# Optimization experiments

Measured on AMD Instinct MI355X. Metric: run time of the kernel, lower is better.

The kernel has to match this reference:

```python
import jax, jax.numpy as jnp
import numpy as np

EPS = 1e-7
MAX_NORM = 1.0 - 1e-3  # projection radius of the unit Poincare ball (c=1)
ALPHA = 0.2            # LeakyReLU negative slope
NEG_INF = -9e15


def _proj(x, max_norm=MAX_NORM):
    # Project points back inside the Poincare ball along the last dim.
    norm = jnp.clip(jnp.linalg.norm(x, axis=-1, keepdims=True), EPS)
    return jnp.where(norm > max_norm, x / norm * max_norm, x)


def _logmap0(x):
    # Log map at the origin of the Poincare ball, c = 1.
    norm = jnp.clip(jnp.linalg.norm(x, axis=-1, keepdims=True), EPS, 1.0 - EPS)
    return jnp.arctanh(norm) * x / norm


def _expmap0(v):
    # Exp map at the origin of the Poincare ball, c = 1.
    norm = jnp.clip(jnp.linalg.norm(v, axis=-1, keepdims=True), EPS)
    return jnp.tanh(norm) * v / norm


def setup_inputs() -> dict:
    key = jax.random.key(0)
    k1, k2, k3 = jax.random.split(key, 3)
    N, D = 12288, 128
    # points strictly inside the ball: ||x|| ~ 0.01*sqrt(128) ~ 0.11 < 1
    x = jax.random.normal(k1, (N, D), dtype=jnp.float32) * 0.01
    adj = jax.random.randint(k2, (N, N), 0, 2, dtype=jnp.int32)
    # attention vector a, as in init: N(0, 0.2) then proj(a, 0.9) row-wise
    a = jax.random.normal(k3, (2 * D, 1), dtype=jnp.float32) * 0.2
    a = _proj(a, 0.9)
    return {"x": x, "adj": adj, "a": a}


def reference(x, adj, a):
    D = a.shape[0] // 2
    x_tan = _logmap0(x)                       # [N, D]
    wh1 = x_tan @ a[:D]                       # [N, 1]
    wh2 = x_tan @ a[D:]                       # [N, 1]
    e = jax.nn.leaky_relu(wh1 + wh2.T, ALPHA)  # [N, N] additive scores
    scores = jnp.where(adj > 0, e, NEG_INF)
    attention = jax.nn.softmax(scores, axis=1)  # dropout omitted (eval mode)
    x_tan_prime = attention @ x_tan            # [N, D]
    return _proj(_expmap0(x_tan_prime))
```

## Files before the change

kernel.cpp:

```cpp
#include <hip/hip_runtime.h>
#include <math.h>

#define NN 12288
#define DD 128
#define EPSF 1e-7f
#define MAXNORM (1.0f - 1e-3f)
#define CSPLIT 4
#define CCOLS (NN / CSPLIT)
#define CSTEPS (CCOLS / 128)
#define BITS_U64_PER_ROW (NN / 64)

typedef __attribute__((ext_vector_type(8))) short short8_t;
typedef __attribute__((ext_vector_type(4))) float float4_t;
typedef unsigned short ushort_t;
typedef unsigned long long u64_t;

__device__ __forceinline__ unsigned short f2bf(float f) {
    unsigned int u = __builtin_bit_cast(unsigned int, f);
    unsigned int r = u + 0x7FFFu + ((u >> 16) & 1u);
    return (unsigned short)(r >> 16);
}

__global__ __launch_bounds__(128) void prep_kernel(
    const float* __restrict__ x, const float* __restrict__ a,
    ushort_t* __restrict__ xtb,
    float* __restrict__ wh1, float* __restrict__ wh2)
{
    const int r = blockIdx.x;
    const int t = threadIdx.x;
    const float xv = x[r * DD + t];
    const float a1 = a[t];
    const float a2 = a[DD + t];
    float s0 = xv * xv, s1 = xv * a1, s2 = xv * a2;
    #pragma unroll
    for (int o = 32; o > 0; o >>= 1) {
        s0 += __shfl_xor(s0, o);
        s1 += __shfl_xor(s1, o);
        s2 += __shfl_xor(s2, o);
    }
    __shared__ float red[6];
    const int w = t >> 6;
    if ((t & 63) == 0) { red[w * 3 + 0] = s0; red[w * 3 + 1] = s1; red[w * 3 + 2] = s2; }
    __syncthreads();
    const float sumsq = red[0] + red[3];
    const float d1    = red[1] + red[4];
    const float d2    = red[2] + red[5];
    const float nraw  = sqrtf(sumsq);
    const float nrm   = fminf(fmaxf(nraw, EPSF), 1.0f - EPSF);
    const float scale = atanhf(nrm) / nrm;
    xtb[(size_t)r * DD + t] = f2bf(xv * scale);
    if (t == 0) {
        wh1[r] = scale * d1;
        wh2[r] = scale * d2;
    }
}

__global__ __launch_bounds__(256) void swizzle_kernel(
    const ushort_t* __restrict__ xtb, ushort_t* __restrict__ xtB)
{
    __shared__ ushort_t raw[32 * 136];
    const int C = blockIdx.x;
    const int t = threadIdx.x;
    #pragma unroll
    for (int p = 0; p < 2; ++p) {
        const int idx = p * 256 + t;
        const int j = idx >> 4, cell = idx & 15;
        const uint4 v = *(const uint4*)(xtb + (size_t)(C * 32 + j) * DD + cell * 8);
        *(uint4*)&raw[j * 136 + cell * 8] = v;
    }
    __syncthreads();
    #pragma unroll
    for (int p = 0; p < 2; ++p) {
        const int oc = p * 256 + t;
        const int dt = oc >> 6;
        const int l6 = oc & 63;
        const int l15 = l6 & 15, q = l6 >> 4;
        short8_t v;
        #pragma unroll
        for (int e = 0; e < 8; ++e)
            v[e] = (short)raw[(q * 8 + e) * 136 + dt * 16 + l15];
        *(short8_t*)(xtB + (size_t)C * 4096 + oc * 8) = v;
    }
}

__global__ __launch_bounds__(256) void bitify_kernel(
    const int* __restrict__ adj, u64_t* __restrict__ bits)
{
    const int i = blockIdx.x;
    const int w = threadIdx.x >> 6;
    const int lane = threadIdx.x & 63;
    const int* rp = adj + (size_t)i * NN;
    #pragma unroll 8
    for (int k = 0; k < BITS_U64_PER_ROW / 4; ++k) {
        const int word = w * (BITS_U64_PER_ROW / 4) + k;
        const int v = rp[word * 64 + lane];
        const u64_t b = __ballot(v > 0);
        if (lane == 0) bits[(size_t)i * BITS_U64_PER_ROW + word] = b;
    }
}

__global__ __launch_bounds__(256, 3) void attn_kernel(
    const u64_t* __restrict__ bits,
    const ushort_t* __restrict__ xtB,
    const float* __restrict__ wh1, const float* __restrict__ wh2,
    float* __restrict__ pout, float* __restrict__ plsum)
{
    __shared__ __align__(16) float wh2_lds[CCOLS];

    const int t = threadIdx.x;
    const int w = t >> 6, lane = t & 63;
    const int l15 = lane & 15, quad = lane >> 4;
    const int cy = blockIdx.y;
    const int jcol0 = cy * CCOLS;
    const int rowbase = blockIdx.x * 64 + w * 16;

    #pragma unroll
    for (int m = 0; m < CCOLS / 256; ++m)
        wh2_lds[m * 256 + t] = wh2[jcol0 + m * 256 + t];
    const float wh1i = wh1[rowbase + l15];
    __syncthreads();

    const uint4* bitp = (const uint4*)bits
                      + (size_t)(rowbase + l15) * (NN / 128) + cy * CSTEPS;
    const ushort_t* Bbase = xtB + (size_t)(jcol0 >> 5) * 4096 + (size_t)lane * 8;

    float4_t acc[8];
    #pragma unroll
    for (int dt = 0; dt < 8; ++dt) acc[dt] = (float4_t)0.0f;
    float lsum = 0.0f;

    auto process = [&](int st, const uint4& A) {
        const int sb = st * 128;
        #pragma unroll
        for (int kc = 0; kc < 4; ++kc) {
            const unsigned word = (kc == 0) ? A.x : (kc == 1) ? A.y
                                : (kc == 2) ? A.z : A.w;
            const unsigned wq = (word >> (quad * 8)) & 0xFFu;
            const int wbase = sb + kc * 32 + quad * 8;
            const float4 Wa = *(const float4*)&wh2_lds[wbase];
            const float4 Wb = *(const float4*)&wh2_lds[wbase + 4];
            const float u0 = wh1i + Wa.x, u1 = wh1i + Wa.y;
            const float u2 = wh1i + Wa.z, u3 = wh1i + Wa.w;
            const float u4 = wh1i + Wb.x, u5 = wh1i + Wb.y;
            const float u6 = wh1i + Wb.z, u7 = wh1i + Wb.w;
            const float p0 = (wq & 1u)   ? __expf(fmaxf(u0, 0.2f * u0)) : 0.0f;
            const float p1 = (wq & 2u)   ? __expf(fmaxf(u1, 0.2f * u1)) : 0.0f;
            const float p2 = (wq & 4u)   ? __expf(fmaxf(u2, 0.2f * u2)) : 0.0f;
            const float p3 = (wq & 8u)   ? __expf(fmaxf(u3, 0.2f * u3)) : 0.0f;
            const float p4 = (wq & 16u)  ? __expf(fmaxf(u4, 0.2f * u4)) : 0.0f;
            const float p5 = (wq & 32u)  ? __expf(fmaxf(u5, 0.2f * u5)) : 0.0f;
            const float p6 = (wq & 64u)  ? __expf(fmaxf(u6, 0.2f * u6)) : 0.0f;
            const float p7 = (wq & 128u) ? __expf(fmaxf(u7, 0.2f * u7)) : 0.0f;
            lsum += ((p0 + p1) + (p2 + p3)) + ((p4 + p5) + (p6 + p7));
            short8_t af;
            af[0] = (short)f2bf(p0); af[1] = (short)f2bf(p1);
            af[2] = (short)f2bf(p2); af[3] = (short)f2bf(p3);
            af[4] = (short)f2bf(p4); af[5] = (short)f2bf(p5);
            af[6] = (short)f2bf(p6); af[7] = (short)f2bf(p7);
            const ushort_t* Bp = Bbase + (size_t)(st * 4 + kc) * 4096;
            #pragma unroll
            for (int dt = 0; dt < 8; ++dt) {
                const short8_t Bf = *(const short8_t*)(Bp + dt * 512);
                acc[dt] = __builtin_amdgcn_mfma_f32_16x16x32_bf16(af, Bf, acc[dt], 0, 0, 0);
            }
        }
    };

    uint4 A0 = bitp[0], A1 = bitp[1], A2;
    #pragma unroll 1
    for (int st = 0; st < CSTEPS; st += 3) {
        A2 = bitp[st + 2];
        process(st, A0);
        if (st + 3 < CSTEPS) A0 = bitp[st + 3];
        process(st + 1, A1);
        if (st + 4 < CSTEPS) A1 = bitp[st + 4];
        process(st + 2, A2);
    }

    float v = lsum;
    v += __shfl_xor(v, 16);
    v += __shfl_xor(v, 32);
    if (quad == 0) plsum[(size_t)cy * NN + rowbase + l15] = v;
    #pragma unroll
    for (int dt = 0; dt < 8; ++dt)
        #pragma unroll
        for (int reg = 0; reg < 4; ++reg)
            pout[((size_t)cy * NN + rowbase + quad * 4 + reg) * DD + dt * 16 + l15]
                = acc[dt][reg];
}

__global__ __launch_bounds__(128) void reduce_kernel(
    const float* __restrict__ pout, const float* __restrict__ plsum,
    float* __restrict__ out)
{
    const int i = blockIdx.x;
    const int t = threadIdx.x;
    float v = 0.0f;
    #pragma unroll
    for (int s = 0; s < CSPLIT; ++s) v += pout[((size_t)s * NN + i) * DD + t];
    float ls = 0.0f;
    #pragma unroll
    for (int s = 0; s < CSPLIT; ++s) ls += plsum[(size_t)s * NN + i];
    v /= ls;
    float ss = v * v;
    #pragma unroll
    for (int o = 1; o < 64; o <<= 1) ss += __shfl_xor(ss, o);
    __shared__ float r2[2];
    if ((t & 63) == 0) r2[t >> 6] = ss;
    __syncthreads();
    const float total = r2[0] + r2[1];
    const float nraw = sqrtf(total);
    const float nv   = fmaxf(nraw, EPSF);
    const float th   = tanhf(nv);
    const float ysc  = th / nv;
    const float nyr  = ysc * nraw;
    const float ny   = fmaxf(nyr, EPSF);
    const float psc  = (ny > MAXNORM) ? (MAXNORM / ny) : 1.0f;
    const float os   = ysc * psc;
    out[(size_t)i * DD + t] = v * os;
}

extern "C" void kernel_launch(void* const* d_in, const int* in_sizes, int n_in,
                              void* d_out, int out_size, void* d_ws, size_t ws_size,
                              hipStream_t stream) {
    const float* x   = (const float*)d_in[0];
    const int*   adj = (const int*)d_in[1];
    const float* a   = (const float*)d_in[2];
    float* out = (float*)d_out;

    char* ws = (char*)d_ws;
    ushort_t* xtb = (ushort_t*)ws;  ws += (size_t)NN * DD * sizeof(ushort_t);
    ushort_t* xtB = (ushort_t*)ws;  ws += (size_t)NN * DD * sizeof(ushort_t);
    float* wh1 = (float*)ws;        ws += NN * sizeof(float);
    float* wh2 = (float*)ws;        ws += NN * sizeof(float);
    float* plsum = (float*)ws;      ws += (size_t)CSPLIT * NN * sizeof(float);
    float* pout  = (float*)ws;      ws += (size_t)CSPLIT * NN * DD * sizeof(float);
    u64_t* bits  = (u64_t*)ws;

    prep_kernel<<<NN, 128, 0, stream>>>(x, a, xtb, wh1, wh2);
    swizzle_kernel<<<NN / 32, 256, 0, stream>>>(xtb, xtB);
    bitify_kernel<<<NN, 256, 0, stream>>>(adj, bits);
    attn_kernel<<<dim3(NN / 64, CSPLIT), 256, 0, stream>>>(
        bits, xtB, wh1, wh2, pout, plsum);
    reduce_kernel<<<NN, 128, 0, stream>>>(pout, plsum, out);
}
```

Measured before the change: 1.029 ms.

## Stage xt B tiles through double-buffered LDS shared by all waves

```diff
diff --git a/kernel.cpp b/kernel.cpp
--- a/kernel.cpp
+++ b/kernel.cpp
@@ -99,12 +99,14 @@
     }
 }
 
-__global__ __launch_bounds__(256, 3) void attn_kernel(
+__global__ __launch_bounds__(256, 2) void attn_kernel(
     const u64_t* __restrict__ bits,
     const ushort_t* __restrict__ xtB,
     const float* __restrict__ wh1, const float* __restrict__ wh2,
     float* __restrict__ pout, float* __restrict__ plsum)
 {
+    __shared__ __align__(16) ushort_t Bl0[128 * DD];
+    __shared__ __align__(16) ushort_t Bl1[128 * DD];
     __shared__ __align__(16) float wh2_lds[CCOLS];
 
     const int t = threadIdx.x;
@@ -118,25 +120,36 @@
     for (int m = 0; m < CCOLS / 256; ++m)
         wh2_lds[m * 256 + t] = wh2[jcol0 + m * 256 + t];
     const float wh1i = wh1[rowbase + l15];
-    __syncthreads();
 
     const uint4* bitp = (const uint4*)bits
                       + (size_t)(rowbase + l15) * (NN / 128) + cy * CSTEPS;
-    const ushort_t* Bbase = xtB + (size_t)(jcol0 >> 5) * 4096 + (size_t)lane * 8;
+    const uint4* Bsrc = (const uint4*)(xtB + (size_t)(jcol0 >> 5) * 4096);
 
     float4_t acc[8];
     #pragma unroll
     for (int dt = 0; dt < 8; ++dt) acc[dt] = (float4_t)0.0f;
     float lsum = 0.0f;
 
-    auto process = [&](int st, const uint4& A) {
-        const int sb = st * 128;
+    uint4 sr[8];
+
+    auto stage_load = [&](int st) {
+        const uint4* sp = Bsrc + (size_t)st * 2048 + t;
+        #pragma unroll
+        for (int r = 0; r < 8; ++r) sr[r] = sp[r * 256];
+    };
+    auto stage_write = [&](ushort_t* buf) {
+        uint4* d = (uint4*)buf + t;
+        #pragma unroll
+        for (int r = 0; r < 8; ++r) d[r * 256] = sr[r];
+    };
+
+    auto compute = [&](int st, const ushort_t* buf, const uint4 M) {
         #pragma unroll
         for (int kc = 0; kc < 4; ++kc) {
-            const unsigned word = (kc == 0) ? A.x : (kc == 1) ? A.y
-                                : (kc == 2) ? A.z : A.w;
+            const unsigned word = (kc == 0) ? M.x : (kc == 1) ? M.y
+                                : (kc == 2) ? M.z : M.w;
             const unsigned wq = (word >> (quad * 8)) & 0xFFu;
-            const int wbase = sb + kc * 32 + quad * 8;
+            const int wbase = st * 128 + kc * 32 + quad * 8;
             const float4 Wa = *(const float4*)&wh2_lds[wbase];
             const float4 Wb = *(const float4*)&wh2_lds[wbase + 4];
             const float u0 = wh1i + Wa.x, u1 = wh1i + Wa.y;
@@ -157,7 +170,7 @@
             af[2] = (short)f2bf(p2); af[3] = (short)f2bf(p3);
             af[4] = (short)f2bf(p4); af[5] = (short)f2bf(p5);
             af[6] = (short)f2bf(p6); af[7] = (short)f2bf(p7);
-            const ushort_t* Bp = Bbase + (size_t)(st * 4 + kc) * 4096;
+            const ushort_t* Bp = buf + kc * 4096 + lane * 8;
             #pragma unroll
             for (int dt = 0; dt < 8; ++dt) {
                 const short8_t Bf = *(const short8_t*)(Bp + dt * 512);
@@ -166,15 +179,26 @@
         }
     };
 
-    uint4 A0 = bitp[0], A1 = bitp[1], A2;
+    stage_load(0);
+    stage_write(Bl0);
+    uint4 Mc = bitp[0];
+    __syncthreads();
+
     #pragma unroll 1
-    for (int st = 0; st < CSTEPS; st += 3) {
-        A2 = bitp[st + 2];
-        process(st, A0);
-        if (st + 3 < CSTEPS) A0 = bitp[st + 3];
-        process(st + 1, A1);
-        if (st + 4 < CSTEPS) A1 = bitp[st + 4];
-        process(st + 2, A2);
+    for (int st0 = 0; st0 < CSTEPS; st0 += 2) {
+        if (st0 + 1 < CSTEPS) stage_load(st0 + 1);
+        const uint4 Mn1 = (st0 + 1 < CSTEPS) ? bitp[st0 + 1] : Mc;
+        compute(st0, Bl0, Mc);
+        Mc = Mn1;
+        if (st0 + 1 < CSTEPS) stage_write(Bl1);
+        __syncthreads();
+        if (st0 + 1 >= CSTEPS) break;
+        if (st0 + 2 < CSTEPS) stage_load(st0 + 2);
+        const uint4 Mn2 = (st0 + 2 < CSTEPS) ? bitp[st0 + 2] : Mc;
+        compute(st0 + 1, Bl1, Mc);
+        Mc = Mn2;
+        if (st0 + 2 < CSTEPS) stage_write(Bl0);
+        __syncthreads();
     }
 
     float v = lsum;
```

Result: slower. 1.059 ms (+3.0%).

## Stage shared B tiles into LDS via global_load_lds across waves

Applied to the files above, without the earlier changes.

```diff
diff --git a/kernel.cpp b/kernel.cpp
--- a/kernel.cpp
+++ b/kernel.cpp
@@ -5,9 +5,10 @@
 #define DD 128
 #define EPSF 1e-7f
 #define MAXNORM (1.0f - 1e-3f)
-#define CSPLIT 4
+#define CSPLIT 8
 #define CCOLS (NN / CSPLIT)
 #define CSTEPS (CCOLS / 128)
+#define SLABS (CSTEPS / 2)
 #define BITS_U64_PER_ROW (NN / 64)
 
 typedef __attribute__((ext_vector_type(8))) short short8_t;
@@ -99,12 +100,13 @@
     }
 }
 
-__global__ __launch_bounds__(256, 3) void attn_kernel(
+__global__ __launch_bounds__(256, 2) void attn_kernel(
     const u64_t* __restrict__ bits,
     const ushort_t* __restrict__ xtB,
     const float* __restrict__ wh1, const float* __restrict__ wh2,
     float* __restrict__ pout, float* __restrict__ plsum)
 {
+    __shared__ __align__(16) ushort_t B_lds[256 * DD];
     __shared__ __align__(16) float wh2_lds[CCOLS];
 
     const int t = threadIdx.x;
@@ -118,25 +120,35 @@
     for (int m = 0; m < CCOLS / 256; ++m)
         wh2_lds[m * 256 + t] = wh2[jcol0 + m * 256 + t];
     const float wh1i = wh1[rowbase + l15];
-    __syncthreads();
 
     const uint4* bitp = (const uint4*)bits
                       + (size_t)(rowbase + l15) * (NN / 128) + cy * CSTEPS;
-    const ushort_t* Bbase = xtB + (size_t)(jcol0 >> 5) * 4096 + (size_t)lane * 8;
+    const uint4* Bsrc = (const uint4*)(xtB + (size_t)(jcol0 >> 5) * 4096);
 
     float4_t acc[8];
     #pragma unroll
     for (int dt = 0; dt < 8; ++dt) acc[dt] = (float4_t)0.0f;
     float lsum = 0.0f;
 
-    auto process = [&](int st, const uint4& A) {
-        const int sb = st * 128;
+    auto stage = [&](int sl) {
+        const uint4* gp = Bsrc + (size_t)sl * 4096 + (size_t)w * 64 + lane;
+        char* lb = (char*)B_lds + (size_t)w * 64 * 16;
+        #pragma unroll
+        for (int m = 0; m < 16; ++m) {
+            __builtin_amdgcn_global_load_lds(
+                (const __attribute__((address_space(1))) unsigned int*)(gp + m * 256),
+                (__attribute__((address_space(3))) unsigned int*)(lb + (size_t)m * 256 * 16),
+                16, 0, 0);
+        }
+    };
+
+    auto compute = [&](int st, int par, const uint4 M) {
         #pragma unroll
         for (int kc = 0; kc < 4; ++kc) {
-            const unsigned word = (kc == 0) ? A.x : (kc == 1) ? A.y
-                                : (kc == 2) ? A.z : A.w;
+            const unsigned word = (kc == 0) ? M.x : (kc == 1) ? M.y
+                                : (kc == 2) ? M.z : M.w;
             const unsigned wq = (word >> (quad * 8)) & 0xFFu;
-            const int wbase = sb + kc * 32 + quad * 8;
+            const int wbase = st * 128 + kc * 32 + quad * 8;
             const float4 Wa = *(const float4*)&wh2_lds[wbase];
             const float4 Wb = *(const float4*)&wh2_lds[wbase + 4];
             const float u0 = wh1i + Wa.x, u1 = wh1i + Wa.y;
@@ -157,7 +169,7 @@
             af[2] = (short)f2bf(p2); af[3] = (short)f2bf(p3);
             af[4] = (short)f2bf(p4); af[5] = (short)f2bf(p5);
             af[6] = (short)f2bf(p6); af[7] = (short)f2bf(p7);
-            const ushort_t* Bp = Bbase + (size_t)(st * 4 + kc) * 4096;
+            const ushort_t* Bp = B_lds + (par * 4 + kc) * 4096 + lane * 8;
             #pragma unroll
             for (int dt = 0; dt < 8; ++dt) {
                 const short8_t Bf = *(const short8_t*)(Bp + dt * 512);
@@ -166,15 +178,19 @@
         }
     };
 
-    uint4 A0 = bitp[0], A1 = bitp[1], A2;
+    uint4 Mc = bitp[0];
+
     #pragma unroll 1
-    for (int st = 0; st < CSTEPS; st += 3) {
-        A2 = bitp[st + 2];
-        process(st, A0);
-        if (st + 3 < CSTEPS) A0 = bitp[st + 3];
-        process(st + 1, A1);
-        if (st + 4 < CSTEPS) A1 = bitp[st + 4];
-        process(st + 2, A2);
+    for (int sl = 0; sl < SLABS; ++sl) {
+        const int st0 = sl * 2;
+        __syncthreads();
+        stage(sl);
+        __syncthreads();
+        const uint4 Mn = bitp[st0 + 1];
+        compute(st0 + 0, 0, Mc);
+        const uint4 Mn2 = (st0 + 2 < CSTEPS) ? bitp[st0 + 2] : Mn;
+        compute(st0 + 1, 1, Mn);
+        Mc = Mn2;
     }
 
     float v = lsum;
```

Result: faster. 951.5 us (-7.5%).
